# Performance work log

Hardware: AMD Instinct MI355X
Metric: run time of the kernel (lower is better)

Reference implementation:

```python
import jax, jax.numpy as jnp
import numpy as np
from jax import lax

T = 512
CHUNK = 64
H = W = 28
C = 4
D_MODEL = H * W * C  # 3136
D_HIDDEN = 512
ALPHA = 0.9
ETA0 = 0.1
P = 2.0
EPS = 1e-6


def setup_inputs() -> dict:
    key = jax.random.key(0)
    ks = jax.random.split(key, 8)
    x = jax.random.normal(ks[0], (T, C, H, W), dtype=jnp.float32)
    conv_k_w = jax.random.normal(ks[1], (3, 3, C, C), dtype=jnp.float32) / 6.0  # lecun-ish: fan_in=36
    conv_v_w = jax.random.normal(ks[2], (3, 3, C, C), dtype=jnp.float32) / 6.0
    conv_k_b = jnp.zeros((C,), jnp.float32)
    conv_v_b = jnp.zeros((C,), jnp.float32)
    rms_k_scale = jnp.ones((C,), jnp.float32)
    rms_v_scale = jnp.ones((C,), jnp.float32)
    W1 = jax.random.normal(ks[3], (D_MODEL, D_HIDDEN), dtype=jnp.float32) / np.sqrt(D_MODEL).astype(np.float32)
    b1 = jnp.zeros((D_HIDDEN,), jnp.float32)
    W2 = jax.random.normal(ks[4], (D_HIDDEN, D_MODEL), dtype=jnp.float32) / np.sqrt(D_HIDDEN).astype(np.float32)
    b2 = jnp.zeros((D_MODEL,), jnp.float32)
    return {"x": x, "conv_k_w": conv_k_w, "conv_k_b": conv_k_b,
            "conv_v_w": conv_v_w, "conv_v_b": conv_v_b,
            "rms_k_scale": rms_k_scale, "rms_v_scale": rms_v_scale,
            "W1": W1, "b1": b1, "W2": W2, "b2": b2}


def _conv(x_nhwc, w, b):
    y = lax.conv_general_dilated(x_nhwc, w, window_strides=(1, 1), padding='SAME',
                                 dimension_numbers=('NHWC', 'HWIO', 'NHWC'))
    return y + b


def _rmsnorm(z, scale):
    inv = lax.rsqrt(jnp.mean(z * z, axis=-1, keepdims=True) + EPS)
    return z * inv * scale


def _mlp(params, k):
    w1, bb1, w2, bb2 = params
    return jax.nn.gelu(k @ w1 + bb1) @ w2 + bb2


def reference(x, conv_k_w, conv_k_b, conv_v_w, conv_v_b, rms_k_scale, rms_v_scale, W1, b1, W2, b2):
    t = x.shape[0]
    xh = jnp.transpose(x, (0, 2, 3, 1))  # [T,H,W,C]
    nk = _rmsnorm(_conv(xh, conv_k_w, conv_k_b), rms_k_scale).reshape(t, -1)  # [T, D_MODEL]
    nv = _rmsnorm(_conv(xh, conv_v_w, conv_v_b), rms_v_scale).reshape(t, -1)

    params0 = (W1, b1, W2, b2)

    def loss_per_token(params, k, v):
        pred = _mlp(params, k)
        return jnp.sum(jnp.abs(pred - v) ** P)

    etas = ETA0 * ALPHA ** jnp.arange(CHUNK, dtype=jnp.float32)
    betas = ALPHA ** jnp.arange(CHUNK, dtype=jnp.float32)
    weights = etas * (betas[-1] / betas)  # [CHUNK]

    n_chunks = t // CHUNK
    Kc = nk.reshape(n_chunks, CHUNK, D_MODEL)
    Vc = nv.reshape(n_chunks, CHUNK, D_MODEL)

    def chunk_body(params, kv):
        K, V = kv
        # per-token parameter grads: leaves have leading CHUNK axis
        grads = jax.vmap(jax.grad(loss_per_token), in_axes=(None, 0, 0))(params, K, V)
        new_params = jax.tree.map(
            lambda p, g: p - jnp.tensordot(weights, g, axes=((0,), (0,))), params, grads)
        Y = _mlp(new_params, K)  # recall on keys with updated fast weights
        return new_params, Y

    _, Y_chunks = lax.scan(chunk_body, params0, (Kc, Vc))
    Y = Y_chunks.reshape(t, D_MODEL)
    return Y.reshape(t, C, H, W)
```

## Files before the change

### kernel.cpp

```cpp
#include <hip/hip_runtime.h>
#include <math.h>

#define DM 3136
#define DH 512

typedef __attribute__((ext_vector_type(8))) short bf16x8;
typedef __attribute__((ext_vector_type(4))) float f32x4;

__device__ __forceinline__ ushort f2bf(float f) {
  union { float f; unsigned u; } v; v.f = f;
  unsigned r = v.u + 0x7FFFu + ((v.u >> 16) & 1u);
  return (ushort)(r >> 16);
}

#define MICRO_4x4 \
    acc[0][0] += a.x*b.x; acc[0][1] += a.x*b.y; acc[0][2] += a.x*b.z; acc[0][3] += a.x*b.w; \
    acc[1][0] += a.y*b.x; acc[1][1] += a.y*b.y; acc[1][2] += a.y*b.z; acc[1][3] += a.y*b.w; \
    acc[2][0] += a.z*b.x; acc[2][1] += a.z*b.y; acc[2][2] += a.z*b.z; acc[2][3] += a.z*b.w; \
    acc[3][0] += a.w*b.x; acc[3][1] += a.w*b.y; acc[3][2] += a.w*b.z; acc[3][3] += a.w*b.w;

__device__ __forceinline__ void gelu_both(float xx, float& g, float& gp) {
  const float c = 0.7978845608028654f;
  const float a = 0.044715f;
  float x2 = xx * xx;
  float u = c * (xx + a * xx * x2);
  float t = tanhf(u);
  g  = 0.5f * xx * (1.f + t);
  gp = 0.5f * (1.f + t) + 0.5f * xx * (1.f - t * t) * c * (1.f + 3.f * a * x2);
}
__device__ __forceinline__ float gelu_only(float xx) {
  const float c = 0.7978845608028654f;
  const float a = 0.044715f;
  float u = c * (xx + a * xx * xx * xx);
  return 0.5f * xx * (1.f + tanhf(u));
}

__device__ __forceinline__ void nt64_core(
    const ushort* __restrict__ A, int lda,
    const ushort* __restrict__ B, int ldb,
    int ksteps, f32x4* acc) {
  int lane = threadIdx.x & 63;
  int wv = threadIdx.x >> 6;
  int qr = wv >> 1, qc = wv & 1;
  int lr = lane & 15;
  int lk = (lane >> 4) << 3;
  const ushort* pa0 = A + (size_t)(qr * 32 + lr) * lda + lk;
  const ushort* pa1 = pa0 + (size_t)16 * lda;
  const ushort* pb0 = B + (size_t)(qc * 32 + lr) * ldb + lk;
  const ushort* pb1 = pb0 + (size_t)16 * ldb;
  bf16x8 a0 = *(const bf16x8*)pa0;
  bf16x8 a1 = *(const bf16x8*)pa1;
  bf16x8 b0 = *(const bf16x8*)pb0;
  bf16x8 b1 = *(const bf16x8*)pb1;
  for (int s = 0; s < ksteps; ++s) {
    int sn = (s + 1 < ksteps) ? (s + 1) * 32 : s * 32;
    bf16x8 na0 = *(const bf16x8*)(pa0 + sn);
    bf16x8 na1 = *(const bf16x8*)(pa1 + sn);
    bf16x8 nb0 = *(const bf16x8*)(pb0 + sn);
    bf16x8 nb1 = *(const bf16x8*)(pb1 + sn);
    acc[0] = __builtin_amdgcn_mfma_f32_16x16x32_bf16(a0, b0, acc[0], 0, 0, 0);
    acc[1] = __builtin_amdgcn_mfma_f32_16x16x32_bf16(a0, b1, acc[1], 0, 0, 0);
    acc[2] = __builtin_amdgcn_mfma_f32_16x16x32_bf16(a1, b0, acc[2], 0, 0, 0);
    acc[3] = __builtin_amdgcn_mfma_f32_16x16x32_bf16(a1, b1, acc[3], 0, 0, 0);
    a0 = na0; a1 = na1; b0 = nb0; b1 = nb1;
  }
}

__device__ __forceinline__ void nt64_store(const f32x4* acc, float* __restrict__ dst, int ldc) {
  int lane = threadIdx.x & 63, wv = threadIdx.x >> 6;
  int r0 = (wv >> 1) * 32 + ((lane >> 4) << 2);
  int c0 = (wv & 1) * 32 + (lane & 15);
  #pragma unroll
  for (int r = 0; r < 4; ++r) {
    dst[(size_t)(r0 + r) * ldc + c0]           = acc[0][r];
    dst[(size_t)(r0 + r) * ldc + c0 + 16]      = acc[1][r];
    dst[(size_t)(r0 + r + 16) * ldc + c0]      = acc[2][r];
    dst[(size_t)(r0 + r + 16) * ldc + c0 + 16] = acc[3][r];
  }
}

__device__ __forceinline__ void dw_epilogue256(
    const f32x4* acc, int n0, const float* __restrict__ Vn,
    const float* __restrict__ b2in, float wc2,
    ushort* __restrict__ Dwb_o, ushort* __restrict__ Dwt_o,
    float* __restrict__ b2out, float* smem) {
  int lane = threadIdx.x & 63, wvv = threadIdx.x >> 6;
  int qr = wvv >> 1, qc = wvv & 1;
  int r0 = qr * 32 + ((lane >> 4) << 2);
  int c0 = qc * 32 + (lane & 15);
  float csum[2] = {0.f, 0.f};
  #pragma unroll
  for (int r = 0; r < 4; ++r) {
    #pragma unroll
    for (int p = 0; p < 4; ++p) {
      int m = r0 + r + ((p >> 1) ? 16 : 0);
      int dl = c0 + ((p & 1) ? 16 : 0);
      int d = n0 + dl;
      float dw = wc2 * (acc[p][r] + b2in[d] - Vn[(size_t)m * DM + d]);
      ushort db = f2bf(dw);
      Dwb_o[(size_t)m * DM + d] = db;
      Dwt_o[(size_t)d * 64 + m] = db;
      csum[p & 1] += dw;
    }
  }
  int slot = qr * 4 + ((lane >> 4) & 3);
  smem[(size_t)c0 * 8 + slot] = csum[0];
  smem[(size_t)(c0 + 16) * 8 + slot] = csum[1];
  __syncthreads();
  if (threadIdx.x < 64) {
    float s = 0.f;
    #pragma unroll
    for (int q = 0; q < 8; ++q) s += smem[threadIdx.x * 8 + q];
    b2out[n0 + threadIdx.x] = b2in[n0 + threadIdx.x] - s;
  }
}

__global__ __launch_bounds__(256) void conv_rms(
    const float* __restrict__ x,
    const float* __restrict__ wk, const float* __restrict__ bk,
    const float* __restrict__ wv, const float* __restrict__ bv,
    const float* __restrict__ sk, const float* __restrict__ sv,
    const float* __restrict__ W1, ushort* __restrict__ w1tb,
    const float* __restrict__ W2, ushort* __restrict__ W2b0, ushort* __restrict__ W2tb0,
    ushort* __restrict__ nkb, float* __restrict__ nv) {
  __shared__ float smem[4160];
  int tid = threadIdx.x;
  if (blockIdx.x >= 1960) {
    int t = blockIdx.x - 1960;
    int d0 = (t % 49) * 64, h0 = (t / 49) * 64;
    int c = tid & 63, rq = tid >> 6;
    #pragma unroll
    for (int q = 0; q < 16; ++q) {
      int r = q * 4 + rq;
      float v = W2[(size_t)(h0 + r) * DM + d0 + c];
      smem[r * 65 + c] = v;
      W2b0[(size_t)(h0 + r) * DM + d0 + c] = f2bf(v);
    }
    __syncthreads();
    #pragma unroll
    for (int q = 0; q < 16; ++q) {
      int r = q * 4 + rq;
      W2tb0[(size_t)(d0 + r) * DH + h0 + c] = f2bf(smem[c * 65 + r]);
    }
    return;
  }
  if (blockIdx.x >= 1568) {
    int t = blockIdx.x - 1568;
    int d0 = (t % 49) * 64, h0 = (t / 49) * 64;
    int c = tid & 63, rq = tid >> 6;
    #pragma unroll
    for (int q = 0; q < 16; ++q) {
      int r = q * 4 + rq;
      smem[r * 65 + c] = W1[(size_t)(d0 + r) * 512 + h0 + c];
    }
    __syncthreads();
    #pragma unroll
    for (int q = 0; q < 16; ++q) {
      int r = q * 4 + rq;
      w1tb[(size_t)(h0 + r) * 3136 + d0 + c] = f2bf(smem[c * 65 + r]);
    }
    return;
  }
  float* swk = smem;
  float* swv = smem + 144;
  float* sb  = smem + 288;
  if (tid < 144) { swk[tid] = wk[tid]; swv[tid] = wv[tid]; }
  if (tid < 4) {
    sb[tid] = bk[tid]; sb[4 + tid] = bv[tid];
    sb[8 + tid] = sk[tid]; sb[12 + tid] = sv[tid];
  }
  __syncthreads();
  int idx = blockIdx.x * 256 + tid;
  int t = idx / 784, hw = idx - t * 784;
  int h = hw / 28, w = hw - h * 28;
  float ak[4], av[4];
  #pragma unroll
  for (int c = 0; c < 4; ++c) { ak[c] = sb[c]; av[c] = sb[4 + c]; }
  const float* xt = x + (size_t)t * DM;
  for (int kh = 0; kh < 3; ++kh) {
    int ih = h + kh - 1;
    if (ih < 0 || ih >= 28) continue;
    for (int kw = 0; kw < 3; ++kw) {
      int iw = w + kw - 1;
      if (iw < 0 || iw >= 28) continue;
      int base = (kh * 3 + kw) * 16;
      #pragma unroll
      for (int ci = 0; ci < 4; ++ci) {
        float xv = xt[ci * 784 + ih * 28 + iw];
        #pragma unroll
        for (int co = 0; co < 4; ++co) {
          ak[co] += xv * swk[base + ci * 4 + co];
          av[co] += xv * swv[base + ci * 4 + co];
        }
      }
    }
  }
  float mk = (ak[0]*ak[0] + ak[1]*ak[1] + ak[2]*ak[2] + ak[3]*ak[3]) * 0.25f + 1e-6f;
  float mv = (av[0]*av[0] + av[1]*av[1] + av[2]*av[2] + av[3]*av[3]) * 0.25f + 1e-6f;
  float ik = 1.f / sqrtf(mk), iv = 1.f / sqrtf(mv);
  ushort4 ok = { f2bf(ak[0]*ik*sb[8]), f2bf(ak[1]*ik*sb[9]),
                 f2bf(ak[2]*ik*sb[10]), f2bf(ak[3]*ik*sb[11]) };
  float4 ov = { av[0]*iv*sb[12], av[1]*iv*sb[13], av[2]*iv*sb[14], av[3]*iv*sb[15] };
  *(ushort4*)&nkb[(size_t)idx * 4] = ok;
  *(float4*)&nv[(size_t)idx * 4] = ov;
}

__global__ __launch_bounds__(256) void u1_kernel(
    const ushort* __restrict__ nkb, const ushort* __restrict__ w1tb,
    float* __restrict__ KKsl, float* __restrict__ Hb_sl) {
  f32x4 acc[4] = {{0.f,0.f,0.f,0.f},{0.f,0.f,0.f,0.f},{0.f,0.f,0.f,0.f},{0.f,0.f,0.f,0.f}};
  int job = blockIdx.x;
  if (job < 448) {
    int s = job % 7;
    int t = job / 7;
    int m0 = (t >> 3) * 64, n0 = (t & 7) * 64;
    nt64_core(nkb + (size_t)m0 * DM + s * 448, DM, w1tb + (size_t)n0 * DM + s * 448, DM, 14, acc);
    nt64_store(acc, Hb_sl + (size_t)s * 262144 + (size_t)m0 * 512 + n0, 512);
  } else {
    int j2 = job - 448;
    int p = j2 / 7, s = j2 % 7;
    int c = 0;
    while ((c + 1) * (c + 2) / 2 <= p) ++c;
    int j = p - c * (c + 1) / 2;
    nt64_core(nkb + (size_t)c * 64 * DM + s * 448, DM, nkb + (size_t)j * 64 * DM + s * 448, DM, 14, acc);
    nt64_store(acc, KKsl + ((size_t)p * 7 + s) * 4096, 64);
  }
}

__global__ __launch_bounds__(256) void u2_kernel(
    const float* __restrict__ KKsl, const float* __restrict__ Hb_sl,
    float* __restrict__ KKf, float* __restrict__ Hbase,
    const float* __restrict__ b1,
    float* __restrict__ Hh, ushort* __restrict__ Gb, ushort* __restrict__ Gtb,
    float* __restrict__ Gp) {
  int i = blockIdx.x * 256 + threadIdx.x;
  if (i < 147456) {
    int pair = i >> 12, e = i & 4095;
    float s = 0.f;
    #pragma unroll
    for (int t = 0; t < 7; ++t) s += KKsl[((size_t)pair * 7 + t) * 4096 + e];
    KKf[i] = s;
  } else {
    int j = i - 147456;
    float s = 0.f;
    #pragma unroll
    for (int t = 0; t < 7; ++t) s += Hb_sl[(size_t)t * 262144 + j];
    Hbase[j] = s;
    if (j < 32768) {
      Hh[j] = s;
      float g, gp;
      gelu_both(s + b1[j & 511], g, gp);
      Gb[j] = f2bf(g);
      Gtb[(j & 511) * 64 + (j >> 9)] = f2bf(g);
      Gp[j] = gp;
    }
  }
}

__device__ __forceinline__ void hs_corr_job(
    const float* __restrict__ KK, const float* __restrict__ Ewj,
    float* __restrict__ dst, int bx, float* smem) {
  float* As = smem;
  float* Bs = smem + 4096;
  int tid = threadIdx.x;
  int n0 = bx * 64;
  {
    int m = tid >> 2, ib = (tid & 3) * 16;
    #pragma unroll
    for (int q = 0; q < 4; ++q) {
      float4 v = *(const float4*)(KK + m * 64 + ib + q * 4);
      As[(ib + q*4 + 0)*64 + m] = v.x;
      As[(ib + q*4 + 1)*64 + m] = v.y;
      As[(ib + q*4 + 2)*64 + m] = v.z;
      As[(ib + q*4 + 3)*64 + m] = v.w;
    }
    int kr = tid >> 4, nn = (tid & 15) * 4;
    #pragma unroll
    for (int q = 0; q < 4; ++q)
      *(float4*)&Bs[(kr + q*16)*64 + nn] = *(const float4*)(Ewj + (size_t)(kr + q*16) * DH + n0 + nn);
  }
  __syncthreads();
  int tx = tid & 15, ty = tid >> 4;
  float acc[4][4] = {{0.f}};
  #pragma unroll 16
  for (int kk = 0; kk < 64; ++kk) {
    float4 a = *(const float4*)&As[kk*64 + ty * 4];
    float4 b = *(const float4*)&Bs[kk*64 + tx * 4];
    MICRO_4x4
  }
  #pragma unroll
  for (int r = 0; r < 4; ++r) {
    float4 v = { acc[r][0], acc[r][1], acc[r][2], acc[r][3] };
    *(float4*)&dst[(ty*4 + r) * DH + n0 + tx*4] = v;
  }
}

__global__ __launch_bounds__(256) void pred0_kernel(
    const ushort* __restrict__ Gb0, const ushort* __restrict__ W2tb0,
    const float* __restrict__ V, const float* __restrict__ b2in, float wc2,
    float* __restrict__ b2out, ushort* __restrict__ Dwb_o, ushort* __restrict__ Dwt_o) {
  __shared__ float smem[512];
  f32x4 acc[4] = {{0.f,0.f,0.f,0.f},{0.f,0.f,0.f,0.f},{0.f,0.f,0.f,0.f},{0.f,0.f,0.f,0.f}};
  int n0 = blockIdx.x * 64;
  nt64_core(Gb0, 512, W2tb0 + (size_t)n0 * 512, 512, 16, acc);
  dw_epilogue256(acc, n0, V, b2in, wc2, Dwb_o, Dwt_o, b2out, smem);
}

__global__ __launch_bounds__(256) void p4w2_kernel(
    const ushort* __restrict__ Dwb, const ushort* __restrict__ Dwtb,
    const ushort* __restrict__ Gtb, const ushort* __restrict__ W2b_c,
    const float* __restrict__ W2c, float* __restrict__ W2n,
    ushort* __restrict__ W2b_n, ushort* __restrict__ W2tb_n,
    float* __restrict__ Esl) {
  f32x4 acc[4] = {{0.f,0.f,0.f,0.f},{0.f,0.f,0.f,0.f},{0.f,0.f,0.f,0.f},{0.f,0.f,0.f,0.f}};
  int b = blockIdx.x;
  if (b < 56) {
    int s = b % 7, nt = b / 7;
    nt64_core(Dwb + s * 448, DM, W2b_c + (size_t)nt * 64 * DM + s * 448, DM, 14, acc);
    nt64_store(acc, Esl + (size_t)s * 32768 + nt * 64, 512);
  } else {
    int li = b - 56;
    int d0 = (li % 49) * 64, h0 = (li / 49) * 64;
    nt64_core(Gtb + (size_t)h0 * 64, 64, Dwtb + (size_t)d0 * 64, 64, 2, acc);
    int lane = threadIdx.x & 63, wvv = threadIdx.x >> 6;
    int r0 = (wvv >> 1) * 32 + ((lane >> 4) << 2);
    int c0 = (wvv & 1) * 32 + (lane & 15);
    #pragma unroll
    for (int r = 0; r < 4; ++r) {
      #pragma unroll
      for (int p = 0; p < 4; ++p) {
        int h = h0 + r0 + r + ((p >> 1) ? 16 : 0);
        int d = d0 + c0 + ((p & 1) ? 16 : 0);
        size_t off = (size_t)h * DM + d;
        float w = W2c[off] - acc[p][r];
        W2n[off] = w;
        ushort wb = f2bf(w);
        W2b_n[off] = wb;
        W2tb_n[(size_t)d * DH + h] = wb;
      }
    }
  }
}

__global__ __launch_bounds__(256) void g2hr_kernel(
    const float* __restrict__ KKf, int ch,
    const float* __restrict__ Esl, const float* __restrict__ GpC,
    const float* __restrict__ Hcur, const float* __restrict__ b1e,
    float* __restrict__ b1o, ushort* __restrict__ G2b, float* __restrict__ EwOut,
    const float* __restrict__ Hcorr, const float* __restrict__ Hbase_n,
    float* __restrict__ HhN, ushort* __restrict__ GbN,
    ushort* __restrict__ GtbN, float* __restrict__ GpN) {
  __shared__ float smem[5200];
  int blk = blockIdx.x;
  int tid = threadIdx.x;
  int tri = ch * (ch + 1) / 2;
  if (blk < 32) {
    float* KKs = smem;
    float* Ews = smem + 4160;
    float* b1l = smem + 5184;
    const float* KKcc = KKf + (size_t)(tri + ch) * 4096;
    int n0 = blk * 16;
    #pragma unroll
    for (int q = 0; q < 16; ++q) {
      int e = q * 256 + tid;
      KKs[(e >> 6) * 65 + (e & 63)] = KKcc[e];
    }
    #pragma unroll
    for (int q = 0; q < 4; ++q) {
      int e = q * 256 + tid;
      int i = e >> 4, cc = e & 15;
      size_t off = (size_t)i * 512 + n0 + cc;
      float s = 0.f;
      #pragma unroll
      for (int sl = 0; sl < 7; ++sl) s += Esl[(size_t)sl * 32768 + off];
      Ews[e] = s * GpC[off];
    }
    __syncthreads();
    if (tid < 16) {
      float s = 0.f;
      for (int i = 0; i < 64; ++i) s += Ews[i * 16 + tid];
      b1l[tid] = b1e[n0 + tid] - s;
    }
    __syncthreads();
    #pragma unroll
    for (int q = 0; q < 4; ++q) {
      int e = q * 256 + tid;
      int mrow = e >> 4, cc = e & 15;
      float corr = 0.f;
      #pragma unroll 16
      for (int i = 0; i < 64; ++i) corr += KKs[mrow * 65 + i] * Ews[i * 16 + cc];
      float xx = Hcur[(size_t)mrow * 512 + n0 + cc] - corr + b1l[cc];
      G2b[(size_t)mrow * 512 + n0 + cc] = f2bf(gelu_only(xx));
    }
  } else if (blk < 40) {
    float* Bs = smem;
    int bx = blk - 32;
    int n0 = bx * 64;
    #pragma unroll
    for (int q = 0; q < 16; ++q) {
      int e = q * 256 + tid;
      int k = e >> 6, c = e & 63;
      size_t off = (size_t)k * 512 + n0 + c;
      float s = 0.f;
      #pragma unroll
      for (int sl = 0; sl < 7; ++sl) s += Esl[(size_t)sl * 32768 + off];
      float ew = s * GpC[off];
      Bs[k * 64 + c] = ew;
      EwOut[off] = ew;
    }
    __syncthreads();
    if (tid < 64) {
      float s = 0.f;
      for (int k = 0; k < 64; ++k) s += Bs[k * 64 + tid];
      b1o[n0 + tid] = b1e[n0 + tid] - s;
    }
  } else {
    float* Ewt = smem;
    float* KKs = smem + 1024;
    float* b1l = smem + 2064;
    int bh = blk - 40;
    int m0 = (bh >> 5) * 16;
    int c0 = (bh & 31) * 16;
    #pragma unroll
    for (int q = 0; q < 4; ++q) {
      int e = q * 256 + tid;
      int i = e >> 4, cl = e & 15;
      size_t off = (size_t)i * 512 + c0 + cl;
      float s = 0.f;
      #pragma unroll
      for (int sl = 0; sl < 7; ++sl) s += Esl[(size_t)sl * 32768 + off];
      Ewt[i * 16 + cl] = s * GpC[off];
    }
    const float* KK = KKf + (size_t)((ch + 1) * (ch + 2) / 2 + ch) * 4096;
    #pragma unroll
    for (int q = 0; q < 4; ++q) {
      int e = q * 256 + tid;
      int ml = e >> 6, i = e & 63;
      KKs[ml * 65 + i] = KK[(m0 + ml) * 64 + i];
    }
    __syncthreads();
    if (tid < 16) {
      float s = 0.f;
      for (int i = 0; i < 64; ++i) s += Ewt[i * 16 + tid];
      b1l[tid] = b1e[c0 + tid] - s;
    }
    __syncthreads();
    int ml = tid >> 4, cl = tid & 15;
    int m = m0 + ml, c = c0 + cl;
    float corr = 0.f;
    #pragma unroll 16
    for (int i = 0; i < 64; ++i) corr += KKs[ml * 65 + i] * Ewt[i * 16 + cl];
    size_t off = (size_t)m * 512 + c;
    float s = Hbase_n[off] - corr;
    for (int j = 0; j < ch; ++j) s -= Hcorr[(size_t)j * 32768 + off];
    HhN[off] = s;
    float g, gp;
    gelu_both(s + b1l[cl], g, gp);
    GbN[off] = f2bf(g);
    GtbN[(size_t)c * 64 + m] = f2bf(g);
    GpN[off] = gp;
  }
}

__global__ __launch_bounds__(256) void yp3_kernel(
    const ushort* __restrict__ G2b, const ushort* __restrict__ W2tb,
    const float* __restrict__ b2n, float* __restrict__ out, int t0,
    const ushort* __restrict__ Gnb, const float* __restrict__ Vn, float wc2,
    float* __restrict__ b2out, ushort* __restrict__ Dwb, ushort* __restrict__ Dwtb,
    const float* __restrict__ KKf, int ch,
    const float* __restrict__ Ewst, float* __restrict__ Hcorr) {
  __shared__ float smem[8192];
  int b = blockIdx.x;
  if (b < 49) {
    f32x4 acc[4] = {{0.f,0.f,0.f,0.f},{0.f,0.f,0.f,0.f},{0.f,0.f,0.f,0.f},{0.f,0.f,0.f,0.f}};
    int n0 = b * 64;
    nt64_core(G2b, 512, W2tb + (size_t)n0 * 512, 512, 16, acc);
    int lane = threadIdx.x & 63, wvv = threadIdx.x >> 6;
    int r0 = (wvv >> 1) * 32 + ((lane >> 4) << 2);
    int c0 = (wvv & 1) * 32 + (lane & 15);
    #pragma unroll
    for (int r = 0; r < 4; ++r) {
      #pragma unroll
      for (int p = 0; p < 4; ++p) {
        int m = r0 + r + ((p >> 1) ? 16 : 0);
        int d = n0 + c0 + ((p & 1) ? 16 : 0);
        out[(size_t)(t0 + m) * DM + d] = acc[p][r] + b2n[d];
      }
    }
  } else if (ch < 7 && b < 98) {
    f32x4 acc[4] = {{0.f,0.f,0.f,0.f},{0.f,0.f,0.f,0.f},{0.f,0.f,0.f,0.f},{0.f,0.f,0.f,0.f}};
    int n0 = (b - 49) * 64;
    nt64_core(Gnb, 512, W2tb + (size_t)n0 * 512, 512, 16, acc);
    dw_epilogue256(acc, n0, Vn, b2n, wc2, Dwb, Dwtb, b2out, smem);
  } else {
    int j2 = b - (ch < 7 ? 98 : 49);
    int j = j2 >> 3, bx = j2 & 7;
    int trin = (ch + 2) * (ch + 3) / 2;
    hs_corr_job(KKf + (size_t)(trin + j) * 4096, Ewst + (size_t)j * 32768,
                Hcorr + (size_t)j * 32768, bx, smem);
  }
}

extern "C" void kernel_launch(void* const* d_in, const int* in_sizes, int n_in,
                              void* d_out, int out_size, void* d_ws, size_t ws_size,
                              hipStream_t stream) {
  const float* x  = (const float*)d_in[0];
  const float* wk = (const float*)d_in[1];
  const float* bk = (const float*)d_in[2];
  const float* wv = (const float*)d_in[3];
  const float* bv = (const float*)d_in[4];
  const float* sk = (const float*)d_in[5];
  const float* sv = (const float*)d_in[6];
  const float* W1 = (const float*)d_in[7];
  const float* b1 = (const float*)d_in[8];
  const float* W2 = (const float*)d_in[9];
  const float* b2 = (const float*)d_in[10];
  float* out = (float*)d_out;
  float* ws  = (float*)d_ws;

  ushort* nkb   = (ushort*)ws;
  ushort* w1tb  = (ushort*)(ws + 802816);
  float* nv     = ws + 1605632;
  float* W2A    = nv + 1605632;
  float* W2B    = W2A + 1605632;
  float* bf_base = W2B + 1605632;
  ushort* W2b0  = (ushort*)bf_base;
  ushort* W2tb0 = (ushort*)(bf_base + 802816);
  ushort* W2bA  = (ushort*)(bf_base + 1605632);
  ushort* W2bB  = (ushort*)(bf_base + 2408448);
  ushort* W2tbA = (ushort*)(bf_base + 3211264);
  ushort* W2tbB = (ushort*)(bf_base + 4014080);
  float* Esl    = bf_base + 4816896;
  float* Hb_sl  = Esl + 229376;
  float* KKsl   = Hb_sl + 1835008;
  float* Hbase  = KKsl + 1032192;
  float* KKf    = Hbase + 262144;
  float* HhA    = KKf + 147456;
  float* HhB    = HhA + 32768;
  float* GpA    = HhB + 32768;
  float* GpB    = GpA + 32768;
  ushort* GbA   = (ushort*)(GpB + 32768);
  ushort* GbB   = (ushort*)(GpB + 49152);
  ushort* GtbA  = (ushort*)(GpB + 65536);
  ushort* GtbB  = (ushort*)(GpB + 81920);
  ushort* G2b   = (ushort*)(GpB + 98304);
  ushort* Dwb   = (ushort*)(GpB + 114688);
  ushort* Dwtb  = (ushort*)(GpB + 215040);
  float* Ewst   = GpB + 315392;
  float* Hcorr  = Ewst + 262144;
  float* b1A    = Hcorr + 229376;
  float* b1B    = b1A + 512;
  float* b2A    = b1B + 512;
  float* b2B    = b2A + 3136;

  float* W2buf[2]   = { W2A, W2B };
  ushort* W2bb[2]   = { W2bA, W2bB };
  ushort* W2tbb[2]  = { W2tbA, W2tbB };
  ushort* Gbb[2]    = { GbA, GbB };
  ushort* Gtbb[2]   = { GtbA, GtbB };
  float* Hhb[2]     = { HhA, HhB };
  float* Gpb[2]     = { GpA, GpB };
  float* b1buf[2]   = { b1A, b1B };
  float* b2buf[2]   = { b2A, b2B };

  float wc2 = 2.0f * (float)(0.1 * pow(0.9, 63.0));

  conv_rms<<<2352, 256, 0, stream>>>(x, wk, bk, wv, bv, sk, sv,
                                     W1, w1tb, W2, W2b0, W2tb0, nkb, nv);
  u1_kernel<<<700, 256, 0, stream>>>(nkb, w1tb, KKsl, Hb_sl);
  u2_kernel<<<1600, 256, 0, stream>>>(KKsl, Hb_sl, KKf, Hbase, b1, HhA, GbA, GtbA, GpA);
  pred0_kernel<<<49, 256, 0, stream>>>(GbA, W2tb0, nv, b2, wc2, b2A, Dwb, Dwtb);

  for (int ch = 0; ch < 8; ++ch) {
    const float* b1e  = ch ? b1buf[(ch - 1) & 1] : b1;
    const float* W2c  = ch ? W2buf[(ch - 1) & 1] : W2;
    const ushort* W2b_c = ch ? W2bb[(ch - 1) & 1] : W2b0;

    p4w2_kernel<<<448, 256, 0, stream>>>(
        Dwb, Dwtb, Gtbb[ch & 1], W2b_c, W2c,
        W2buf[ch & 1], W2bb[ch & 1], W2tbb[ch & 1], Esl);
    g2hr_kernel<<<(ch < 7 ? 168 : 32), 256, 0, stream>>>(
        KKf, ch, Esl, Gpb[ch & 1], Hhb[ch & 1], b1e, b1buf[ch & 1],
        G2b, Ewst + (size_t)ch * 32768,
        Hcorr, Hbase + (size_t)((ch + 1) & 7) * 32768,
        Hhb[(ch + 1) & 1], Gbb[(ch + 1) & 1], Gtbb[(ch + 1) & 1], Gpb[(ch + 1) & 1]);
    int g3 = 49 + (ch < 7 ? 49 : 0) + (ch < 6 ? 8 * (ch + 1) : 0);
    yp3_kernel<<<g3, 256, 0, stream>>>(
        G2b, W2tbb[ch & 1], b2buf[ch & 1], out, ch * 64,
        Gbb[(ch + 1) & 1], nv + (size_t)((ch + 1) & 7) * 200704, wc2,
        b2buf[(ch + 1) & 1], Dwb, Dwtb,
        KKf, ch, Ewst, Hcorr);
  }
}
```

Baseline: 352.6 us.

## Fuse per-chunk kernel sequence into one persistent cooperative kernel with grid syncs

The 24 per-chunk launches (three stage kernels for each of eight chunks) are replaced by a single cooperative persistent kernel. It loops over the chunks and stages, dividing work among blocks in grid-stride loops and using grid.sync between stages. The aim is to remove kernel launch gaps and tail effects between small dependent launches. In exchange it relies on cooperative launch support, possibly lower occupancy from the fused kernel's register and shared-memory needs, and grid-wide barrier costs, and it keeps the old launch path as a fallback.

```diff
diff --git a/kernel.cpp b/kernel.cpp
--- a/kernel.cpp
+++ b/kernel.cpp
@@ -1,4 +1,5 @@
 #include <hip/hip_runtime.h>
+#include <hip/hip_cooperative_groups.h>
 #include <math.h>
 
 #define DM 3136
@@ -306,14 +307,15 @@
   dw_epilogue256(acc, n0, V, b2in, wc2, Dwb_o, Dwt_o, b2out, smem);
 }
 
-__global__ __launch_bounds__(256) void p4w2_kernel(
+
+__device__ __forceinline__ void s1_body(
+    int b,
     const ushort* __restrict__ Dwb, const ushort* __restrict__ Dwtb,
     const ushort* __restrict__ Gtb, const ushort* __restrict__ W2b_c,
     const float* __restrict__ W2c, float* __restrict__ W2n,
     ushort* __restrict__ W2b_n, ushort* __restrict__ W2tb_n,
     float* __restrict__ Esl) {
   f32x4 acc[4] = {{0.f,0.f,0.f,0.f},{0.f,0.f,0.f,0.f},{0.f,0.f,0.f,0.f},{0.f,0.f,0.f,0.f}};
-  int b = blockIdx.x;
   if (b < 56) {
     int s = b % 7, nt = b / 7;
     nt64_core(Dwb + s * 448, DM, W2b_c + (size_t)nt * 64 * DM + s * 448, DM, 14, acc);
@@ -342,16 +344,15 @@
   }
 }
 
-__global__ __launch_bounds__(256) void g2hr_kernel(
-    const float* __restrict__ KKf, int ch,
+__device__ __forceinline__ void s2_body(
+    int blk, int ch, float* smem,
+    const float* __restrict__ KKf,
     const float* __restrict__ Esl, const float* __restrict__ GpC,
     const float* __restrict__ Hcur, const float* __restrict__ b1e,
     float* __restrict__ b1o, ushort* __restrict__ G2b, float* __restrict__ EwOut,
     const float* __restrict__ Hcorr, const float* __restrict__ Hbase_n,
     float* __restrict__ HhN, ushort* __restrict__ GbN,
     ushort* __restrict__ GtbN, float* __restrict__ GpN) {
-  __shared__ float smem[5200];
-  int blk = blockIdx.x;
   int tid = threadIdx.x;
   int tri = ch * (ch + 1) / 2;
   if (blk < 32) {
@@ -462,15 +463,15 @@
   }
 }
 
-__global__ __launch_bounds__(256) void yp3_kernel(
+__device__ __forceinline__ void s3_body(
+    int b, int ch, float* smem,
     const ushort* __restrict__ G2b, const ushort* __restrict__ W2tb,
-    const float* __restrict__ b2n, float* __restrict__ out, int t0,
+    const float* __restrict__ b2n, float* __restrict__ out,
     const ushort* __restrict__ Gnb, const float* __restrict__ Vn, float wc2,
     float* __restrict__ b2out, ushort* __restrict__ Dwb, ushort* __restrict__ Dwtb,
-    const float* __restrict__ KKf, int ch,
+    const float* __restrict__ KKf,
     const float* __restrict__ Ewst, float* __restrict__ Hcorr) {
-  __shared__ float smem[8192];
-  int b = blockIdx.x;
+  int t0 = ch * 64;
   if (b < 49) {
     f32x4 acc[4] = {{0.f,0.f,0.f,0.f},{0.f,0.f,0.f,0.f},{0.f,0.f,0.f,0.f},{0.f,0.f,0.f,0.f}};
     int n0 = b * 64;
@@ -498,6 +499,113 @@
     int trin = (ch + 2) * (ch + 3) / 2;
     hs_corr_job(KKf + (size_t)(trin + j) * 4096, Ewst + (size_t)j * 32768,
                 Hcorr + (size_t)j * 32768, bx, smem);
+  }
+}
+
+__global__ __launch_bounds__(256) void p4w2_kernel(
+    const ushort* __restrict__ Dwb, const ushort* __restrict__ Dwtb,
+    const ushort* __restrict__ Gtb, const ushort* __restrict__ W2b_c,
+    const float* __restrict__ W2c, float* __restrict__ W2n,
+    ushort* __restrict__ W2b_n, ushort* __restrict__ W2tb_n,
+    float* __restrict__ Esl) {
+  s1_body(blockIdx.x, Dwb, Dwtb, Gtb, W2b_c, W2c, W2n, W2b_n, W2tb_n, Esl);
+}
+
+__global__ __launch_bounds__(256) void g2hr_kernel(
+    const float* __restrict__ KKf, int ch,
+    const float* __restrict__ Esl, const float* __restrict__ GpC,
+    const float* __restrict__ Hcur, const float* __restrict__ b1e,
+    float* __restrict__ b1o, ushort* __restrict__ G2b, float* __restrict__ EwOut,
+    const float* __restrict__ Hcorr, const float* __restrict__ Hbase_n,
+    float* __restrict__ HhN, ushort* __restrict__ GbN,
+    ushort* __restrict__ GtbN, float* __restrict__ GpN) {
+  __shared__ float smem[8192];
+  s2_body(blockIdx.x, ch, smem, KKf, Esl, GpC, Hcur, b1e, b1o, G2b, EwOut,
+          Hcorr, Hbase_n, HhN, GbN, GtbN, GpN);
+}
+
+__global__ __launch_bounds__(256) void yp3_kernel(
+    const ushort* __restrict__ G2b, const ushort* __restrict__ W2tb,
+    const float* __restrict__ b2n, float* __restrict__ out, int ch,
+    const ushort* __restrict__ Gnb, const float* __restrict__ Vn, float wc2,
+    float* __restrict__ b2out, ushort* __restrict__ Dwb, ushort* __restrict__ Dwtb,
+    const float* __restrict__ KKf,
+    const float* __restrict__ Ewst, float* __restrict__ Hcorr) {
+  __shared__ float smem[8192];
+  s3_body(blockIdx.x, ch, smem, G2b, W2tb, b2n, out, Gnb, Vn, wc2,
+          b2out, Dwb, Dwtb, KKf, Ewst, Hcorr);
+}
+
+struct CLP {
+  const float* KKf;
+  float* Esl;
+  const float* Hbase;
+  float* Hcorr;
+  float* Ewst;
+  float* out;
+  const float* nv;
+  float* HhA; float* HhB;
+  float* GpA; float* GpB;
+  ushort* GbA; ushort* GbB;
+  ushort* GtbA; ushort* GtbB;
+  ushort* G2b;
+  ushort* Dwb; ushort* Dwtb;
+  float* W2A; float* W2B;
+  ushort* W2bA; ushort* W2bB;
+  ushort* W2tbA; ushort* W2tbB;
+  const float* W2_0; const ushort* W2b0c; const ushort* W2tb0c;
+  const float* b1_0; float* b1A; float* b1B;
+  float* b2A; float* b2B;
+  float wc2;
+};
+
+__global__ __launch_bounds__(256, 2) void chunk_kernel(CLP p) {
+  cooperative_groups::grid_group grid = cooperative_groups::this_grid();
+  __shared__ float smem[8192];
+  int G = gridDim.x;
+  for (int ch = 0; ch < 8; ++ch) {
+    const float* b1e = ch ? (((ch - 1) & 1) ? p.b1B : p.b1A) : p.b1_0;
+    const float* W2c = ch ? (((ch - 1) & 1) ? p.W2B : p.W2A) : p.W2_0;
+    const ushort* W2b_c = ch ? (((ch - 1) & 1) ? p.W2bB : p.W2bA) : p.W2b0c;
+    const ushort* Gtb_c = (ch & 1) ? p.GtbB : p.GtbA;
+    float* W2n = (ch & 1) ? p.W2B : p.W2A;
+    ushort* W2b_n = (ch & 1) ? p.W2bB : p.W2bA;
+    ushort* W2tb_n = (ch & 1) ? p.W2tbB : p.W2tbA;
+
+    for (int j = blockIdx.x; j < 448; j += G) {
+      s1_body(j, p.Dwb, p.Dwtb, Gtb_c, W2b_c, W2c, W2n, W2b_n, W2tb_n, p.Esl);
+      __syncthreads();
+    }
+    grid.sync();
+
+    const float* GpC = (ch & 1) ? p.GpB : p.GpA;
+    const float* Hcur = (ch & 1) ? p.HhB : p.HhA;
+    float* b1o = (ch & 1) ? p.b1B : p.b1A;
+    float* HhN = ((ch + 1) & 1) ? p.HhB : p.HhA;
+    ushort* GbN = ((ch + 1) & 1) ? p.GbB : p.GbA;
+    ushort* GtbN = ((ch + 1) & 1) ? p.GtbB : p.GtbA;
+    float* GpN = ((ch + 1) & 1) ? p.GpB : p.GpA;
+    int n2 = (ch < 7) ? 168 : 32;
+    for (int j = blockIdx.x; j < n2; j += G) {
+      s2_body(j, ch, smem, p.KKf, p.Esl, GpC, Hcur, b1e, b1o, p.G2b,
+              p.Ewst + (size_t)ch * 32768, p.Hcorr,
+              p.Hbase + (size_t)((ch + 1) & 7) * 32768, HhN, GbN, GtbN, GpN);
+      __syncthreads();
+    }
+    grid.sync();
+
+    const ushort* W2tb_cur = (ch & 1) ? p.W2tbB : p.W2tbA;
+    const float* b2n = (ch & 1) ? p.b2B : p.b2A;
+    const ushort* Gnb = ((ch + 1) & 1) ? p.GbB : p.GbA;
+    float* b2out = ((ch + 1) & 1) ? p.b2B : p.b2A;
+    int g3 = 49 + (ch < 7 ? 49 : 0) + (ch < 6 ? 8 * (ch + 1) : 0);
+    for (int j = blockIdx.x; j < g3; j += G) {
+      s3_body(j, ch, smem, p.G2b, W2tb_cur, b2n, p.out,
+              Gnb, p.nv + (size_t)((ch + 1) & 7) * 200704, p.wc2,
+              b2out, p.Dwb, p.Dwtb, p.KKf, p.Ewst, p.Hcorr);
+      __syncthreads();
+    }
+    if (ch < 7) grid.sync();
   }
 }
 
@@ -571,24 +679,49 @@
   u2_kernel<<<1600, 256, 0, stream>>>(KKsl, Hb_sl, KKf, Hbase, b1, HhA, GbA, GtbA, GpA);
   pred0_kernel<<<49, 256, 0, stream>>>(GbA, W2tb0, nv, b2, wc2, b2A, Dwb, Dwtb);
 
-  for (int ch = 0; ch < 8; ++ch) {
-    const float* b1e  = ch ? b1buf[(ch - 1) & 1] : b1;
-    const float* W2c  = ch ? W2buf[(ch - 1) & 1] : W2;
-    const ushort* W2b_c = ch ? W2bb[(ch - 1) & 1] : W2b0;
-
-    p4w2_kernel<<<448, 256, 0, stream>>>(
-        Dwb, Dwtb, Gtbb[ch & 1], W2b_c, W2c,
-        W2buf[ch & 1], W2bb[ch & 1], W2tbb[ch & 1], Esl);
-    g2hr_kernel<<<(ch < 7 ? 168 : 32), 256, 0, stream>>>(
-        KKf, ch, Esl, Gpb[ch & 1], Hhb[ch & 1], b1e, b1buf[ch & 1],
-        G2b, Ewst + (size_t)ch * 32768,
-        Hcorr, Hbase + (size_t)((ch + 1) & 7) * 32768,
-        Hhb[(ch + 1) & 1], Gbb[(ch + 1) & 1], Gtbb[(ch + 1) & 1], Gpb[(ch + 1) & 1]);
-    int g3 = 49 + (ch < 7 ? 49 : 0) + (ch < 6 ? 8 * (ch + 1) : 0);
-    yp3_kernel<<<g3, 256, 0, stream>>>(
-        G2b, W2tbb[ch & 1], b2buf[ch & 1], out, ch * 64,
-        Gbb[(ch + 1) & 1], nv + (size_t)((ch + 1) & 7) * 200704, wc2,
-        b2buf[(ch + 1) & 1], Dwb, Dwtb,
-        KKf, ch, Ewst, Hcorr);
-  }
-}
+  CLP cp;
+  cp.KKf = KKf; cp.Esl = Esl; cp.Hbase = Hbase; cp.Hcorr = Hcorr; cp.Ewst = Ewst;
+  cp.out = out; cp.nv = nv;
+  cp.HhA = HhA; cp.HhB = HhB; cp.GpA = GpA; cp.GpB = GpB;
+  cp.GbA = GbA; cp.GbB = GbB; cp.GtbA = GtbA; cp.GtbB = GtbB;
+  cp.G2b = G2b; cp.Dwb = Dwb; cp.Dwtb = Dwtb;
+  cp.W2A = W2A; cp.W2B = W2B; cp.W2bA = W2bA; cp.W2bB = W2bB;
+  cp.W2tbA = W2tbA; cp.W2tbB = W2tbB;
+  cp.W2_0 = W2; cp.W2b0c = W2b0; cp.W2tb0c = W2tb0;
+  cp.b1_0 = b1; cp.b1A = b1A; cp.b1B = b1B;
+  cp.b2A = b2A; cp.b2B = b2B;
+  cp.wc2 = wc2;
+
+  int maxPerCU = 0;
+  if (hipOccupancyMaxActiveBlocksPerMultiprocessor(&maxPerCU, chunk_kernel, 256, 0)
+        != hipSuccess || maxPerCU < 1)
+    maxPerCU = 1;
+  int coopGrid = maxPerCU * 256;
+  if (coopGrid > 448) coopGrid = 448;
+
+  void* kargs[] = { &cp };
+  hipError_t cerr = hipLaunchCooperativeKernel(chunk_kernel, dim3(coopGrid), dim3(256),
+                                               kargs, 0, stream);
+  if (cerr != hipSuccess) {
+    for (int ch = 0; ch < 8; ++ch) {
+      const float* b1e  = ch ? b1buf[(ch - 1) & 1] : b1;
+      const float* W2c  = ch ? W2buf[(ch - 1) & 1] : W2;
+      const ushort* W2b_c = ch ? W2bb[(ch - 1) & 1] : W2b0;
+
+      p4w2_kernel<<<448, 256, 0, stream>>>(
+          Dwb, Dwtb, Gtbb[ch & 1], W2b_c, W2c,
+          W2buf[ch & 1], W2bb[ch & 1], W2tbb[ch & 1], Esl);
+      g2hr_kernel<<<(ch < 7 ? 168 : 32), 256, 0, stream>>>(
+          KKf, ch, Esl, Gpb[ch & 1], Hhb[ch & 1], b1e, b1buf[ch & 1],
+          G2b, Ewst + (size_t)ch * 32768,
+          Hcorr, Hbase + (size_t)((ch + 1) & 7) * 32768,
+          Hhb[(ch + 1) & 1], Gbb[(ch + 1) & 1], Gtbb[(ch + 1) & 1], Gpb[(ch + 1) & 1]);
+      int g3 = 49 + (ch < 7 ? 49 : 0) + (ch < 6 ? 8 * (ch + 1) : 0);
+      yp3_kernel<<<g3, 256, 0, stream>>>(
+          G2b, W2tbb[ch & 1], b2buf[ch & 1], out, ch,
+          Gbb[(ch + 1) & 1], nv + (size_t)((ch + 1) & 7) * 200704, wc2,
+          b2buf[(ch + 1) & 1], Dwb, Dwtb,
+          KKf, Ewst, Hcorr);
+    }
+  }
+}
```

New measurement: 1.227 ms. +247.9%, slower.
